# Kernel tuning notes

Measured on AMD Instinct MI355X. Metric: run time of the kernel, lower is better.

## Reference

```python
import jax, jax.numpy as jnp
import numpy as np

NV = 1_000_000   # number of 'var' nodes
NC = 500_000     # number of 'con' nodes
E = 16_000_000   # number of v2c edges (c2v is the reverse edge set)
H = 10           # n_h_feats


def setup_inputs() -> dict:
    key = jax.random.key(0)
    ks = jax.random.split(key, 24)
    s = 0.1  # weight init scale
    inp = {
        "var_c": jax.random.normal(ks[0], (NV,), jnp.float32),
        "var_x": jax.random.normal(ks[1], (NV,), jnp.float32),
        "con_b": jax.random.normal(ks[2], (NC,), jnp.float32),
        "A": jax.random.uniform(ks[3], (E,), jnp.float32),
        "src": jax.random.randint(ks[4], (E,), 0, NV, jnp.int32),
        "dst": jax.random.randint(ks[5], (E,), 0, NC, jnp.int32),
        # var_emb / con_emb Linear params
        "Wv": jax.random.normal(ks[6], (2, H), jnp.float32) * s,
        "bv": jnp.zeros((H,), jnp.float32),
        "Wc": jax.random.normal(ks[7], (1, H), jnp.float32) * s,
        "bc": jnp.zeros((H,), jnp.float32),
        # conv1 (GraphConv, shared across v2c/c2v) -- note: its output is
        # overwritten in the original forward and never reaches the output
        "W1": jax.random.normal(ks[8], (H, H), jnp.float32) * s,
        "b1": jnp.zeros((H,), jnp.float32),
        # conv2 (GraphConv, shared across v2c/c2v)
        "W2": jax.random.normal(ks[9], (H, H), jnp.float32) * s,
        "b2": jnp.zeros((H,), jnp.float32),
        # output MLP
        "Wo1": jax.random.normal(ks[10], (H, H), jnp.float32) * s,
        "bo1": jnp.zeros((H,), jnp.float32),
        "Wo2": jax.random.normal(ks[11], (H, H), jnp.float32) * s,
        "bo2": jnp.zeros((H,), jnp.float32),
        "Wo3": jax.random.normal(ks[12], (H, 1), jnp.float32) * s,
        "bo3": jnp.zeros((1,), jnp.float32),
    }
    return inp


def _gconv(x_src, W, b, s_idx, d_idx, ew, norm_src, norm_dst, n_dst):
    # DGL GraphConv, norm='both', with edge weights; in==out feats so W first.
    h = (x_src * norm_src) @ W                      # [N_src, H]
    msg = h[s_idx] * ew[:, None]                    # gather + edge weight
    agg = jax.ops.segment_sum(msg, d_idx, num_segments=n_dst)
    return agg * norm_dst + b


def reference(var_c, var_x, con_b, A, src, dst,
              Wv, bv, Wc, bc, W1, b1, W2, b2,
              Wo1, bo1, Wo2, bo2, Wo3, bo3):
    # symmetric norm from UNWEIGHTED degrees (DGL GraphConv norm='both'),
    # clamped at 1. v2c: out-deg(var), in-deg(con); c2v is the reverse.
    ones_e = jnp.ones_like(A)
    deg_v = jnp.clip(jax.ops.segment_sum(ones_e, src, num_segments=NV), 1.0)
    deg_c = jnp.clip(jax.ops.segment_sum(ones_e, dst, num_segments=NC), 1.0)
    norm_v = deg_v[:, None] ** -0.5
    norm_c = deg_c[:, None] ** -0.5

    # node embeddings
    var_feats = jnp.stack([var_c, var_x], axis=1)   # [NV, 2]
    X_var = jax.nn.relu(var_feats @ Wv + bv)        # [NV, H]
    X_con = jax.nn.relu(con_b[:, None] @ Wc + bc)   # [NC, H] (unused by convs: GraphConv ignores dst feats)

    # In the original forward, conv1 outputs (h_con / h_var) are immediately
    # overwritten by conv2 outputs (GraphConv only consumes src features),
    # so only conv2 lies on the effective compute path.
    h_con = jax.nn.relu(_gconv(X_var, W2, b2, src, dst, A, norm_v, norm_c, NC))
    h_var = jax.nn.relu(_gconv(h_con, W2, b2, dst, src, A, norm_c, norm_v, NV))

    h = jax.nn.relu(h_var @ Wo1 + bo1)
    h = jax.nn.relu(h @ Wo2 + bo2)
    logit = h @ Wo3 + bo3                           # [NV, 1]
    # dgl.readout_nodes(op='mean', ntype='var'), single graph -> [1, 1]
    return jnp.mean(logit, axis=0, keepdims=True)
```

## Files before the change

### kernel.cpp

```cpp
#include <hip/hip_runtime.h>

#define HF 10
#define ST 16
#define BST 16
#define SLC 256
#define NBINS 2048
#define VPB 512
#define TILE 12288
#define NBD 1024
#define DSH 9
#define CPB 512
#define TILED 6144


__global__ __launch_bounds__(1024) void k_hist(const int* __restrict__ idx,
                                               unsigned* __restrict__ hist,
                                               long long s_begin, long long s_end,
                                               int per, int shift) {
    __shared__ unsigned l[NBINS];
    int t = threadIdx.x, sl = blockIdx.x;
    for (int b = t; b < NBINS; b += 1024) l[b] = 0u;
    __syncthreads();
    long long s0 = s_begin + (long long)sl * per;
    long long s1 = s0 + per; if (s1 > s_end) s1 = s_end;
    for (long long i = s0 + t; i < s1; i += 1024)
        atomicAdd(&l[((unsigned)idx[i]) >> shift], 1u);
    __syncthreads();
    unsigned* out = hist + (size_t)sl * NBINS;
    for (int b = t; b < NBINS; b += 1024) out[b] = l[b];
}

__global__ void k_coltot(const unsigned* __restrict__ h, unsigned* __restrict__ colT) {
    int b = blockIdx.x * 256 + threadIdx.x;
    unsigned s = 0u;
    for (int sl = 0; sl < SLC; sl++) s += h[(size_t)sl * NBINS + b];
    colT[b] = s;
}

__global__ __launch_bounds__(1024) void k_prefix(const unsigned* __restrict__ colT,
                                                 unsigned* __restrict__ start) {
    __shared__ unsigned p[1024];
    int t = threadIdx.x;
    uint2 v = *(const uint2*)(colT + 2 * t);
    unsigned own = v.x + v.y;
    p[t] = own;
    __syncthreads();
    for (int off = 1; off < 1024; off <<= 1) {
        unsigned u = (t >= off) ? p[t - off] : 0u;
        __syncthreads();
        p[t] += u;
        __syncthreads();
    }
    unsigned e = p[t] - own;
    *(uint2*)(start + 2 * t) = make_uint2(e, e + v.x);
    if (t == 1023) start[NBINS] = p[1023];
}

__global__ void k_offs(unsigned* __restrict__ h, const unsigned* __restrict__ start) {
    int b = blockIdx.x * 256 + threadIdx.x;
    unsigned cur = start[b];
    for (int sl = 0; sl < SLC; sl++) {
        unsigned* cell = h + (size_t)sl * NBINS + b;
        unsigned v = *cell;
        *cell = cur;
        cur += v;
    }
}

__global__ __launch_bounds__(1024) void k_scatS2(
        const int* __restrict__ src, const int* __restrict__ dst,
        const float* __restrict__ A, const unsigned* __restrict__ offs,
        uint2* __restrict__ ebufS, long long E, int per) {
    __shared__ unsigned cur[NBINS];
    __shared__ unsigned th[NBINS];
    __shared__ unsigned tf[NBINS];
    __shared__ unsigned sc[1024];
    __shared__ __align__(16) uint2 buf[TILE];
    int t = threadIdx.x, sl = blockIdx.x;
    const unsigned* o = offs + (size_t)sl * NBINS;
    for (int b = t; b < NBINS; b += 1024) cur[b] = o[b];
    long long s0 = (long long)sl * per;
    long long s1 = s0 + per; if (s1 > E) s1 = E;
    for (long long tb = s0; tb < s1; tb += TILE) {
        int n = (int)((s1 - tb < (long long)TILE) ? (s1 - tb) : (long long)TILE);
        for (int b = t; b < NBINS; b += 1024) th[b] = 0u;
        __syncthreads();
        for (int i = t; i < n; i += 1024)
            atomicAdd(&th[((unsigned)src[tb + i]) >> 9], 1u);
        __syncthreads();
        unsigned a0 = th[2 * t], a1 = th[2 * t + 1];
        unsigned own = a0 + a1;
        sc[t] = own;
        __syncthreads();
        for (int off = 1; off < 1024; off <<= 1) {
            unsigned u = (t >= off) ? sc[t - off] : 0u;
            __syncthreads();
            sc[t] += u;
            __syncthreads();
        }
        unsigned ex = sc[t] - own;
        th[2 * t] = ex;     th[2 * t + 1] = ex + a0;
        tf[2 * t] = ex;     tf[2 * t + 1] = ex + a0;
        __syncthreads();
        for (int i = t; i < n; i += 1024) {
            unsigned s = (unsigned)src[tb + i], d = (unsigned)dst[tb + i];
            float a = A[tb + i];
            unsigned p = atomicAdd(&tf[s >> 9], 1u);
            buf[p] = make_uint2(((s & 511u) << 19) | d, __float_as_uint(a));
        }
        __syncthreads();
        int w = t >> 6, ln = t & 63;
        for (int b = w; b < NBINS; b += 16) {
            unsigned lo = th[b], cnt = tf[b] - lo, gb = cur[b];
            for (unsigned j = ln; j < cnt; j += 64)
                ebufS[gb + j] = buf[lo + j];
        }
        __syncthreads();
        for (int b = t; b < NBINS; b += 1024) cur[b] += tf[b] - th[b];
        __syncthreads();
    }
}

__global__ void k_cntS2(const uint2* __restrict__ ebufS, const unsigned* __restrict__ startS,
                        const float* __restrict__ var_c, const float* __restrict__ var_x,
                        float4* __restrict__ vcx, int NV) {
    __shared__ unsigned cnt[VPB];
    int t = threadIdx.x, b = blockIdx.x;
    cnt[t] = 0u; cnt[t + 256] = 0u;
    __syncthreads();
    unsigned i0 = startS[b], i1 = startS[b + 1];
    for (unsigned i = i0 + t; i < i1; i += 256)
        atomicAdd(&cnt[ebufS[i].x >> 19], 1u);
    __syncthreads();
#pragma unroll
    for (int k = 0; k < 2; k++) {
        int v = b * VPB + k * 256 + t;
        if (v < NV)
            vcx[v] = make_float4(var_c[v], var_x[v],
                                 rsqrtf(fmaxf((float)cnt[k * 256 + t], 1.0f)), 0.0f);
    }
}

__global__ __launch_bounds__(1024) void k_histD2(const uint2* __restrict__ ebufB,
                                                 const unsigned* __restrict__ startS,
                                                 unsigned* __restrict__ hist, int B0, int binsPer) {
    __shared__ unsigned l[NBINS];
    int t = threadIdx.x, sl = blockIdx.x;
    for (int b = t; b < NBINS; b += 1024) l[b] = 0u;
    __syncthreads();
    int b0 = B0 + sl * binsPer;
    unsigned i0 = startS[b0], i1 = startS[b0 + binsPer];
    for (unsigned i = i0 + t; i < i1; i += 1024)
        atomicAdd(&l[(ebufB[i].x & 0x7FFFFu) >> DSH], 1u);
    __syncthreads();
    unsigned* out = hist + (size_t)sl * NBINS;
    for (int b = t; b < NBINS; b += 1024) out[b] = l[b];
}

__global__ __launch_bounds__(1024) void k_scatD3(
        const uint2* __restrict__ ebufB, const unsigned* __restrict__ startS,
        const unsigned* __restrict__ offs, const float4* __restrict__ vcx,
        uint4* __restrict__ ebufD, int B0, int binsPer, unsigned cap) {
    __shared__ unsigned cur[NBD];
    __shared__ unsigned th[NBD], tf[NBD];
    __shared__ unsigned sc[1024];
    __shared__ __align__(16) uint4 buf[TILED];
    int t = threadIdx.x, sl = blockIdx.x;
    const unsigned* o = offs + (size_t)sl * NBINS;
    cur[t] = o[t];
    __syncthreads();
    int b0 = B0 + sl * binsPer;
    for (int bb = 0; bb < binsPer; bb++) {
        int bin = b0 + bb;
        unsigned vbase = ((unsigned)bin) << 9;
        unsigned i0 = startS[bin], i1 = startS[bin + 1];
        for (unsigned tb = i0; tb < i1; tb += TILED) {
            unsigned n = (i1 - tb < (unsigned)TILED) ? (i1 - tb) : (unsigned)TILED;
            th[t] = 0u;
            __syncthreads();
            for (unsigned i = t; i < n; i += 1024)
                atomicAdd(&th[(ebufB[tb + i].x & 0x7FFFFu) >> DSH], 1u);
            __syncthreads();
            unsigned own = th[t];
            sc[t] = own;
            __syncthreads();
            for (int off = 1; off < 1024; off <<= 1) {
                unsigned u = (t >= off) ? sc[t - off] : 0u;
                __syncthreads();
                sc[t] += u;
                __syncthreads();
            }
            unsigned ex = sc[t] - own;
            th[t] = ex; tf[t] = ex;
            __syncthreads();
            for (unsigned i = t; i < n; i += 1024) {
                uint2 kv = ebufB[tb + i];
                unsigned d = kv.x & 0x7FFFFu;
                float4 g = vcx[vbase | (kv.x >> 19)];
                unsigned p = atomicAdd(&tf[d >> DSH], 1u);
                buf[p] = make_uint4(d & (CPB - 1u),
                                    __float_as_uint(__uint_as_float(kv.y) * g.z),
                                    __float_as_uint(g.x), __float_as_uint(g.y));
            }
            __syncthreads();
            int w = t >> 6, ln = t & 63;
            for (int b = w; b < NBD; b += 16) {
                unsigned lo = th[b], cnt = tf[b] - lo, gb = cur[b];
                for (unsigned j = ln; j < cnt; j += 64)
                    if (gb + j < cap) ebufD[gb + j] = buf[lo + j];
            }
            __syncthreads();
            cur[t] += tf[t] - th[t];
            __syncthreads();
        }
    }
}

__global__ __launch_bounds__(1024) void k_scatD(const int* __restrict__ src, const int* __restrict__ dst,
                                                const float* __restrict__ A,
                                                const unsigned* __restrict__ offs,
                                                const float4* __restrict__ vcx,
                                                uint4* __restrict__ ebufD,
                                                long long s_begin, long long s_end, int per) {
    __shared__ unsigned cur[NBINS];
    int t = threadIdx.x, sl = blockIdx.x;
    const unsigned* o = offs + (size_t)sl * NBINS;
    for (int b = t; b < NBINS; b += 1024) cur[b] = o[b];
    __syncthreads();
    long long s0 = s_begin + (long long)sl * per;
    long long s1 = s0 + per; if (s1 > s_end) s1 = s_end;
    for (long long i = s0 + t; i < s1; i += 4096) {
        unsigned sv[4], dv[4]; float av[4]; bool hv[4];
#pragma unroll
        for (int j = 0; j < 4; j++) {
            long long idx = i + (long long)j * 1024;
            hv[j] = idx < s1;
            if (hv[j]) { sv[j] = (unsigned)src[idx]; dv[j] = (unsigned)dst[idx]; av[j] = A[idx]; }
            else       { sv[j] = 0u; dv[j] = 0u; av[j] = 0.0f; }
        }
        float4 g[4];
#pragma unroll
        for (int j = 0; j < 4; j++)
            if (hv[j]) g[j] = vcx[sv[j]];
#pragma unroll
        for (int j = 0; j < 4; j++) {
            if (!hv[j]) continue;
            unsigned pos = atomicAdd(&cur[dv[j] >> DSH], 1u);
            ebufD[pos] = make_uint4(dv[j] & (CPB - 1u), __float_as_uint(av[j] * g[j].z),
                                    __float_as_uint(g[j].x), __float_as_uint(g[j].y));
        }
    }
}

__global__ __launch_bounds__(256) void k_aggD(
        const uint4* __restrict__ ebufD, const unsigned* __restrict__ startD,
        const float* __restrict__ Wv, const float* __restrict__ bv,
        float* __restrict__ bufC, float* __restrict__ deg_c, int NC) {
    __shared__ float acc[CPB * HF];
    __shared__ unsigned cnt[CPB];
    int t = threadIdx.x, b = blockIdx.x;
    for (int i = t; i < CPB * HF; i += 256) acc[i] = 0.0f;
    cnt[t] = 0u; cnt[t + 256] = 0u;
    float wv0[HF], wv1[HF], bvv[HF];
#pragma unroll
    for (int h = 0; h < HF; h++) { wv0[h] = Wv[h]; wv1[h] = Wv[HF + h]; bvv[h] = bv[h]; }
    __syncthreads();
    unsigned i0 = startD[b], i1 = startD[b + 1];
    for (unsigned i = i0 + t; i < i1; i += 256) {
        uint4 kv = ebufD[i];
        unsigned dl = kv.x;
        float anv = __uint_as_float(kv.y);
        float c   = __uint_as_float(kv.z);
        float x   = __uint_as_float(kv.w);
        float* ac = acc + dl * HF;
#pragma unroll
        for (int h = 0; h < HF; h++) {
            float e = fmaxf(fmaf(c, wv0[h], fmaf(x, wv1[h], bvv[h])), 0.0f);
            atomicAdd(ac + h, anv * e);
        }
        atomicAdd(&cnt[dl], 1u);
    }
    __syncthreads();
#pragma unroll
    for (int k = 0; k < 2; k++) {
        int gid = b * CPB + k * 256 + t;
        if (gid < NC) {
            float* row = bufC + (size_t)gid * BST;
#pragma unroll
            for (int h = 0; h < HF; h++) row[h] += acc[(k * 256 + t) * HF + h];
            deg_c[gid] += (float)cnt[k * 256 + t];
        }
    }
}

__global__ void k_conT(float* __restrict__ bufC, const float* __restrict__ deg_c,
                       const float* __restrict__ W2, const float* __restrict__ b2, int NC) {
    __shared__ float sW[HF * HF], sb[HF];
    int t = threadIdx.x;
    if (t < HF * HF) sW[t] = W2[t];
    if (t < HF)      sb[t] = b2[t];
    __syncthreads();
    int i = blockIdx.x * 256 + t;
    if (i >= NC) return;
    float nc = rsqrtf(fmaxf(deg_c[i], 1.0f));
    float* row = bufC + (size_t)i * BST;
    float x[HF];
#pragma unroll
    for (int h = 0; h < HF; h++) x[h] = row[h];
#pragma unroll
    for (int j = 0; j < HF; j++) {
        float a = 0.0f;
#pragma unroll
        for (int k = 0; k < HF; k++) a = fmaf(x[k], sW[k * HF + j], a);
        row[j] = fmaxf(fmaf(a, nc, sb[j]), 0.0f) * nc;
    }
}

__global__ __launch_bounds__(256) void k_aggS(
        const uint2* __restrict__ ebufS, const unsigned* __restrict__ startS,
        const float* __restrict__ bufC, const float4* __restrict__ vcx,
        const float* __restrict__ W2, const float* __restrict__ b2,
        const float* __restrict__ Wo1, const float* __restrict__ bo1,
        const float* __restrict__ Wo2, const float* __restrict__ bo2,
        const float* __restrict__ Wo3, const float* __restrict__ bo3,
        double* __restrict__ gacc, int NV) {
    __shared__ float acc[VPB * HF];
    __shared__ float sW2[HF * HF], sb2[HF], sW1[HF * HF], sb1[HF], sWm[HF * HF], sbm[HF], sW3[HF];
    __shared__ float sb3;
    __shared__ double red[256];
    int t = threadIdx.x, b = blockIdx.x;
    for (int i = t; i < VPB * HF; i += 256) acc[i] = 0.0f;
    if (t < HF * HF) { sW2[t] = W2[t]; sW1[t] = Wo1[t]; sWm[t] = Wo2[t]; }
    if (t < HF)      { sb2[t] = b2[t]; sb1[t] = bo1[t]; sbm[t] = bo2[t]; sW3[t] = Wo3[t]; }
    if (t == 0)      sb3 = bo3[0];
    __syncthreads();
    unsigned i0 = startS[b], i1 = startS[b + 1];
    int grp = t >> 2;
    int q   = t & 3;
    int nq  = (q < 2) ? 4 : (q == 2 ? 2 : 0);
    for (unsigned base = i0; base < i1; base += 64) {
        unsigned e = base + (unsigned)grp;
        bool ok = e < i1;
        uint2 kv = ok ? ebufS[e] : make_uint2(0u, 0u);
        float4 y = make_float4(0.f, 0.f, 0.f, 0.f);
        if (ok) y = *(const float4*)(bufC + (size_t)(kv.x & 0x7FFFFu) * BST + 4 * q);
        if (ok && nq) {
            float a = __uint_as_float(kv.y);
            float* ac = acc + (kv.x >> 19) * HF + 4 * q;
            atomicAdd(ac + 0, a * y.x);
            atomicAdd(ac + 1, a * y.y);
            if (nq == 4) {
                atomicAdd(ac + 2, a * y.z);
                atomicAdd(ac + 3, a * y.w);
            }
        }
    }
    __syncthreads();
    double local = 0.0;
#pragma unroll
    for (int k = 0; k < 2; k++) {
        int v = b * VPB + k * 256 + t;
        if (v < NV) {
            float nv = vcx[v].z;
            float x[HF], hvv[HF], h1[HF], h2[HF];
#pragma unroll
            for (int h = 0; h < HF; h++) x[h] = acc[(k * 256 + t) * HF + h];
#pragma unroll
            for (int j = 0; j < HF; j++) {
                float a = 0.0f;
#pragma unroll
                for (int kk = 0; kk < HF; kk++) a = fmaf(x[kk], sW2[kk * HF + j], a);
                hvv[j] = fmaxf(fmaf(a, nv, sb2[j]), 0.0f);
            }
#pragma unroll
            for (int j = 0; j < HF; j++) {
                float a = sb1[j];
#pragma unroll
                for (int kk = 0; kk < HF; kk++) a = fmaf(hvv[kk], sW1[kk * HF + j], a);
                h1[j] = fmaxf(a, 0.0f);
            }
#pragma unroll
            for (int j = 0; j < HF; j++) {
                float a = sbm[j];
#pragma unroll
                for (int kk = 0; kk < HF; kk++) a = fmaf(h1[kk], sWm[kk * HF + j], a);
                h2[j] = fmaxf(a, 0.0f);
            }
            float logit = sb3;
#pragma unroll
            for (int kk = 0; kk < HF; kk++) logit = fmaf(h2[kk], sW3[kk], logit);
            local += (double)logit;
        }
    }
    red[t] = local;
    __syncthreads();
    for (int s = 128; s > 0; s >>= 1) {
        if (t < s) red[t] += red[t + s];
        __syncthreads();
    }
    if (t == 0) atomicAdd(gacc, red[0]);
}

__global__ void k_out(const double* __restrict__ acc, float* __restrict__ out, int NV) {
    out[0] = (float)(acc[0] / (double)NV);
}


__global__ void k_degree(const int* __restrict__ src, const int* __restrict__ dst,
                         float* __restrict__ deg_v, float* __restrict__ deg_c, int E) {
    int i = blockIdx.x * blockDim.x + threadIdx.x;
    if (i < E) {
        atomicAdd(&deg_v[src[i]], 1.0f);
        atomicAdd(&deg_c[dst[i]], 1.0f);
    }
}

__global__ void k_norm(float* __restrict__ d, int n) {
    int i = blockIdx.x * blockDim.x + threadIdx.x;
    if (i < n) d[i] = 1.0f / sqrtf(fmaxf(d[i], 1.0f));
}

__global__ void k_var_emb(const float* __restrict__ var_c, const float* __restrict__ var_x,
                          const float* __restrict__ norm_v,
                          const float* __restrict__ Wv, const float* __restrict__ bv,
                          const float* __restrict__ W2,
                          float* __restrict__ out, int NV) {
    __shared__ float sWv[2 * HF], sbv[HF], sW2[HF * HF];
    int t = threadIdx.x;
    if (t < 2 * HF) sWv[t] = Wv[t];
    if (t < HF)     sbv[t] = bv[t];
    if (t < HF * HF) sW2[t] = W2[t];
    __syncthreads();
    int i = blockIdx.x * blockDim.x + t;
    if (i >= NV) return;
    float c = var_c[i], x = var_x[i], nv = norm_v[i];
    float e[HF];
#pragma unroll
    for (int h = 0; h < HF; h++)
        e[h] = fmaxf(fmaf(c, sWv[h], fmaf(x, sWv[HF + h], sbv[h])), 0.0f) * nv;
    float* row = out + (size_t)i * ST;
#pragma unroll
    for (int j = 0; j < HF; j++) {
        float acc = 0.0f;
#pragma unroll
        for (int k = 0; k < HF; k++) acc = fmaf(e[k], sW2[k * HF + j], acc);
        row[j] = acc;
    }
}

__global__ void k_edge(const int* __restrict__ gidx, const int* __restrict__ didx,
                       const float* __restrict__ A,
                       const float* __restrict__ h, float* __restrict__ agg, int E) {
    int tid = blockIdx.x * blockDim.x + threadIdx.x;
    int e = tid / 5;
    if (e >= E) return;
    int q = tid - e * 5;
    int s = gidx[e], d = didx[e];
    float a = A[e];
    const float2 m = *(const float2*)(h + (size_t)s * ST + 2 * q);
    float* o = agg + (size_t)d * ST + 2 * q;
    atomicAdd(o,     m.x * a);
    atomicAdd(o + 1, m.y * a);
}

__global__ void k_con(float* __restrict__ buf, const float* __restrict__ norm_c,
                      const float* __restrict__ W2, const float* __restrict__ b2, int NC) {
    __shared__ float sW2[HF * HF], sb2[HF];
    int t = threadIdx.x;
    if (t < HF * HF) sW2[t] = W2[t];
    if (t < HF)      sb2[t] = b2[t];
    __syncthreads();
    int i = blockIdx.x * blockDim.x + t;
    if (i >= NC) return;
    float nc = norm_c[i];
    float* row = buf + (size_t)i * ST;
    float hc[HF];
#pragma unroll
    for (int h = 0; h < HF; h++)
        hc[h] = fmaxf(fmaf(row[h], nc, sb2[h]), 0.0f) * nc;
#pragma unroll
    for (int j = 0; j < HF; j++) {
        float acc = 0.0f;
#pragma unroll
        for (int k = 0; k < HF; k++) acc = fmaf(hc[k], sW2[k * HF + j], acc);
        row[j] = acc;
    }
}

__global__ void k_final(const float* __restrict__ agg_v, const float* __restrict__ norm_v,
                        const float* __restrict__ b2,
                        const float* __restrict__ Wo1, const float* __restrict__ bo1,
                        const float* __restrict__ Wo2, const float* __restrict__ bo2,
                        const float* __restrict__ Wo3, const float* __restrict__ bo3,
                        double* __restrict__ acc, int NV) {
    __shared__ float sb2[HF], sW1[HF * HF], sb1[HF], sW2m[HF * HF], sb2m[HF], sW3[HF];
    __shared__ float sb3;
    __shared__ double red[256];
    int t = threadIdx.x;
    if (t < HF)      sb2[t]  = b2[t];
    if (t < HF * HF) sW1[t]  = Wo1[t];
    if (t < HF)      sb1[t]  = bo1[t];
    if (t < HF * HF) sW2m[t] = Wo2[t];
    if (t < HF)      sb2m[t] = bo2[t];
    if (t < HF)      sW3[t]  = Wo3[t];
    if (t == 0)      sb3     = bo3[0];
    __syncthreads();
    int i = blockIdx.x * blockDim.x + t;
    double local = 0.0;
    if (i < NV) {
        float nv = norm_v[i];
        const float* row = agg_v + (size_t)i * ST;
        float v[HF], h1[HF], h2[HF];
#pragma unroll
        for (int h = 0; h < HF; h++) v[h] = fmaxf(fmaf(row[h], nv, sb2[h]), 0.0f);
#pragma unroll
        for (int j = 0; j < HF; j++) {
            float a = sb1[j];
#pragma unroll
            for (int k = 0; k < HF; k++) a = fmaf(v[k], sW1[k * HF + j], a);
            h1[j] = fmaxf(a, 0.0f);
        }
#pragma unroll
        for (int j = 0; j < HF; j++) {
            float a = sb2m[j];
#pragma unroll
            for (int k = 0; k < HF; k++) a = fmaf(h1[k], sW2m[k * HF + j], a);
            h2[j] = fmaxf(a, 0.0f);
        }
        float logit = sb3;
#pragma unroll
        for (int k = 0; k < HF; k++) logit = fmaf(h2[k], sW3[k], logit);
        local = (double)logit;
    }
    red[t] = local;
    __syncthreads();
    for (int s = 128; s > 0; s >>= 1) {
        if (t < s) red[t] += red[t + s];
        __syncthreads();
    }
    if (t == 0) atomicAdd(acc, red[0]);
}


extern "C" void kernel_launch(void* const* d_in, const int* in_sizes, int n_in,
                              void* d_out, int out_size, void* d_ws, size_t ws_size,
                              hipStream_t stream) {
    const float* var_c = (const float*)d_in[0];
    const float* var_x = (const float*)d_in[1];
    const float* A   = (const float*)d_in[3];
    const int*   src = (const int*)d_in[4];
    const int*   dst = (const int*)d_in[5];
    const float* Wv  = (const float*)d_in[6];
    const float* bv  = (const float*)d_in[7];
    const float* W2  = (const float*)d_in[12];
    const float* b2  = (const float*)d_in[13];
    const float* Wo1 = (const float*)d_in[14];
    const float* bo1 = (const float*)d_in[15];
    const float* Wo2 = (const float*)d_in[16];
    const float* bo2 = (const float*)d_in[17];
    const float* Wo3 = (const float*)d_in[18];
    const float* bo3 = (const float*)d_in[19];

    const int NV = in_sizes[0];
    const int NC = in_sizes[2];
    const int E  = in_sizes[3];

    long long EcMaxUsed = 0;
    auto layout_bytes = [&](int nDc, bool binchunk, size_t* offs_out) -> size_t {
        size_t off = 0;
        auto alloc = [&](size_t bytes, int slot) {
            if (offs_out) offs_out[slot] = off;
            off = (off + bytes + 255) & ~(size_t)255;
        };
        long long ec;
        if (binchunk) {
            long long vspan = (long long)(NBINS / nDc) * VPB;
            if (vspan > NV) vspan = NV;
            ec = ((long long)E * vspan) / NV + (long long)E / 64 + 1024;
            if (ec > E) ec = E;
        } else {
            ec = ((long long)E + nDc - 1) / nDc;
        }
        EcMaxUsed = ec;
        alloc((size_t)NC * BST * 4, 0);
        alloc((size_t)NV * 16, 1);
        alloc((size_t)NC * 4, 2);
        alloc((size_t)SLC * NBINS * 4, 3);
        alloc((size_t)SLC * NBINS * 4, 4);
        alloc((size_t)NBINS * 4, 5);
        alloc((size_t)(NBINS + 1) * 4, 6);
        alloc((size_t)(NBINS + 1) * 4, 7);
        alloc(8, 8);
        alloc((size_t)E * 8, 9);
        alloc((size_t)ec * 16, 10);
        return off;
    };

    int nD = 0;
    bool binc = false;
    size_t offs[11];
    for (int cand : {4, 8, 16}) {
        if (layout_bytes(cand, true, nullptr) <= ws_size) { nD = cand; binc = true; break; }
    }
    if (nD == 0) {
        for (int cand = 2; cand <= 16; cand++)
            if (layout_bytes(cand, false, nullptr) <= ws_size) { nD = cand; break; }
    }
    bool fast = (nD > 0) && (NV <= (1 << 20)) && (NC <= (1 << 19)) && (E > 0);

    char* ws = (char*)d_ws;
    if (fast) {
        layout_bytes(nD, binc, offs);
        const long long EcMax = EcMaxUsed;
        float*    bufC   = (float*)(ws + offs[0]);
        float4*   vcx    = (float4*)(ws + offs[1]);
        float*    deg_c  = (float*)(ws + offs[2]);
        unsigned* hS     = (unsigned*)(ws + offs[3]);
        unsigned* hD     = (unsigned*)(ws + offs[4]);
        unsigned* colT   = (unsigned*)(ws + offs[5]);
        unsigned* startS = (unsigned*)(ws + offs[6]);
        unsigned* startD = (unsigned*)(ws + offs[7]);
        double*   gacc   = (double*)(ws + offs[8]);
        uint2*    ebufS  = (uint2*)(ws + offs[9]);
        uint4*    ebufD  = (uint4*)(ws + offs[10]);

        const int perS = (int)(((long long)E + SLC - 1) / SLC);
        const int NB_S = (NV + VPB - 1) / VPB;
        const int NB_C = (NC + 255) >> 8;
        const int NB_C2 = (NC + CPB - 1) / CPB;

        hipMemsetAsync(bufC,  0, (size_t)NC * BST * 4, stream);
        hipMemsetAsync(deg_c, 0, (size_t)NC * 4, stream);
        hipMemsetAsync(gacc,  0, 8, stream);

        k_hist<<<SLC, 1024, 0, stream>>>(src, hS, 0, E, perS, 9);
        k_coltot<<<NBINS / 256, 256, 0, stream>>>(hS, colT);
        k_prefix<<<1, 1024, 0, stream>>>(colT, startS);
        k_offs<<<NBINS / 256, 256, 0, stream>>>(hS, startS);
        k_scatS2<<<SLC, 1024, 0, stream>>>(src, dst, A, hS, ebufS, E, perS);

        k_cntS2<<<NB_S, 256, 0, stream>>>(ebufS, startS, var_c, var_x, vcx, NV);

        if (binc) {
            const int binsChunk = NBINS / nD;
            const int binsPer   = (binsChunk + SLC - 1) / SLC;
            for (int c = 0; c < nD; c++) {
                int B0 = c * binsChunk;
                k_histD2<<<SLC, 1024, 0, stream>>>(ebufS, startS, hD, B0, binsPer);
                k_coltot<<<NBINS / 256, 256, 0, stream>>>(hD, colT);
                k_prefix<<<1, 1024, 0, stream>>>(colT, startD);
                k_offs<<<NBINS / 256, 256, 0, stream>>>(hD, startD);
                k_scatD3<<<SLC, 1024, 0, stream>>>(ebufS, startS, hD, vcx, ebufD,
                                                   B0, binsPer, (unsigned)EcMax);
                k_aggD<<<NB_C2, 256, 0, stream>>>(ebufD, startD, Wv, bv, bufC, deg_c, NC);
            }
        } else {
            const int perD = (int)((EcMax + SLC - 1) / SLC);
            for (int c = 0; c < nD; c++) {
                long long cb = (long long)c * EcMax;
                long long ce = cb + EcMax; if (ce > E) ce = E;
                k_hist<<<SLC, 1024, 0, stream>>>(dst, hD, cb, ce, perD, DSH);
                k_coltot<<<NBINS / 256, 256, 0, stream>>>(hD, colT);
                k_prefix<<<1, 1024, 0, stream>>>(colT, startD);
                k_offs<<<NBINS / 256, 256, 0, stream>>>(hD, startD);
                k_scatD<<<SLC, 1024, 0, stream>>>(src, dst, A, hD, vcx, ebufD, cb, ce, perD);
                k_aggD<<<NB_C2, 256, 0, stream>>>(ebufD, startD, Wv, bv, bufC, deg_c, NC);
            }
        }
        k_conT<<<NB_C, 256, 0, stream>>>(bufC, deg_c, W2, b2, NC);

        k_aggS<<<NB_S, 256, 0, stream>>>(ebufS, startS, bufC, vcx, W2, b2,
                                         Wo1, bo1, Wo2, bo2, Wo3, bo3, gacc, NV);
        k_out<<<1, 1, 0, stream>>>(gacc, (float*)d_out, NV);
    } else {
        const int B = 256;
        float* fbufV = (float*)ws;
        float* fbufC = (float*)(ws + (size_t)NV * ST * 4);
        float* deg_v = (float*)(ws + (size_t)(NV + NC) * ST * 4);
        float* deg_c = deg_v + NV;
        size_t acc_off = ((size_t)(NV + NC) * ST * 4 + (size_t)(NV + NC) * 4 + 7) & ~(size_t)7;
        double* acc = (double*)(ws + acc_off);

        hipMemsetAsync(deg_v, 0, (size_t)(NV + NC) * 4, stream);
        hipMemsetAsync(fbufC, 0, (size_t)NC * ST * 4, stream);
        hipMemsetAsync(acc, 0, sizeof(double), stream);

        k_degree<<<(E + B - 1) / B, B, 0, stream>>>(src, dst, deg_v, deg_c, E);
        k_norm<<<(NV + NC + B - 1) / B, B, 0, stream>>>(deg_v, NV + NC);
        k_var_emb<<<(NV + B - 1) / B, B, 0, stream>>>(var_c, var_x, deg_v, Wv, bv, W2, fbufV, NV);

        long long tE = (long long)E * 5;
        k_edge<<<(int)((tE + B - 1) / B), B, 0, stream>>>(src, dst, A, fbufV, fbufC, E);
        k_con<<<(NC + B - 1) / B, B, 0, stream>>>(fbufC, deg_c, W2, b2, NC);

        hipMemsetAsync(fbufV, 0, (size_t)NV * ST * 4, stream);
        k_edge<<<(int)((tE + B - 1) / B), B, 0, stream>>>(dst, src, A, fbufC, fbufV, E);

        k_final<<<(NV + B - 1) / B, B, 0, stream>>>(fbufV, deg_v, b2, Wo1, bo1, Wo2, bo2, Wo3, bo3, acc, NV);
        k_out<<<1, 1, 0, stream>>>(acc, (float*)d_out, NV);
    }
}
```

Baseline: 2.626 ms.

## Widen destination bins, merge per-slice bins into tiles, use wave-shuffle scan

Destination bucketing now uses 512 bins of 1024 constraints instead of 1024 bins of 512, and the in-block scatter tile grows. k_scatD4 handles all of a slice's source bins as one contiguous range and recovers each edge's source bin by comparing against the bin boundaries. It replaces the 1024-wide barrier-heavy Hillis-Steele scan with a wave-level shuffle scan and flattens the write-out so each thread copies records directly. k_aggD now has 1024 constraints per block (40 KB shared accumulator), masks the local index itself, and exits early on empty blocks. The goal is fewer barriers, fewer underfilled tiles and more coalesced writes, at the cost of more shared memory per block (possibly lower occupancy) and a per-edge boundary search loop.

New measurement: 2.477 ms. 5.7% less time.

```diff
diff --git a/kernel.cpp b/kernel.cpp
--- a/kernel.cpp
+++ b/kernel.cpp
@@ -7,10 +7,10 @@
 #define NBINS 2048
 #define VPB 512
 #define TILE 12288
-#define NBD 1024
-#define DSH 9
-#define CPB 512
-#define TILED 6144
+#define NBD 512
+#define DSH 10
+#define CPB 1024
+#define TILED 7424
 
 
 __global__ __launch_bounds__(1024) void k_hist(const int* __restrict__ idx,
@@ -143,13 +143,17 @@
 
 __global__ __launch_bounds__(1024) void k_histD2(const uint2* __restrict__ ebufB,
                                                  const unsigned* __restrict__ startS,
-                                                 unsigned* __restrict__ hist, int B0, int binsPer) {
+                                                 unsigned* __restrict__ hist,
+                                                 int B0, int binsPer, int binsChunk) {
     __shared__ unsigned l[NBINS];
     int t = threadIdx.x, sl = blockIdx.x;
     for (int b = t; b < NBINS; b += 1024) l[b] = 0u;
     __syncthreads();
     int b0 = B0 + sl * binsPer;
-    unsigned i0 = startS[b0], i1 = startS[b0 + binsPer];
+    int bend = b0 + binsPer;
+    if (bend > B0 + binsChunk) bend = B0 + binsChunk;
+    unsigned i0 = 0u, i1 = 0u;
+    if (b0 < bend) { i0 = startS[b0]; i1 = startS[bend]; }
     for (unsigned i = i0 + t; i < i1; i += 1024)
         atomicAdd(&l[(ebufB[i].x & 0x7FFFFu) >> DSH], 1u);
     __syncthreads();
@@ -157,62 +161,70 @@
     for (int b = t; b < NBINS; b += 1024) out[b] = l[b];
 }
 
-__global__ __launch_bounds__(1024) void k_scatD3(
+__global__ __launch_bounds__(1024) void k_scatD4(
         const uint2* __restrict__ ebufB, const unsigned* __restrict__ startS,
         const unsigned* __restrict__ offs, const float4* __restrict__ vcx,
-        uint4* __restrict__ ebufD, int B0, int binsPer, unsigned cap) {
-    __shared__ unsigned cur[NBD];
-    __shared__ unsigned th[NBD], tf[NBD];
-    __shared__ unsigned sc[1024];
+        uint4* __restrict__ ebufD, int B0, int binsPer, int binsChunk, unsigned cap) {
+    __shared__ unsigned cur[NBD], th[NBD], tf[NBD];
+    __shared__ unsigned ws[16];
+    __shared__ unsigned bnd[16];
     __shared__ __align__(16) uint4 buf[TILED];
     int t = threadIdx.x, sl = blockIdx.x;
+    int b0 = B0 + sl * binsPer;
+    int bend = b0 + binsPer;
+    if (bend > B0 + binsChunk) bend = B0 + binsChunk;
+    int binsEff = bend - b0;
+    if (binsEff <= 0) return;
     const unsigned* o = offs + (size_t)sl * NBINS;
-    cur[t] = o[t];
-    __syncthreads();
-    int b0 = B0 + sl * binsPer;
-    for (int bb = 0; bb < binsPer; bb++) {
-        int bin = b0 + bb;
-        unsigned vbase = ((unsigned)bin) << 9;
-        unsigned i0 = startS[bin], i1 = startS[bin + 1];
-        for (unsigned tb = i0; tb < i1; tb += TILED) {
-            unsigned n = (i1 - tb < (unsigned)TILED) ? (i1 - tb) : (unsigned)TILED;
-            th[t] = 0u;
-            __syncthreads();
-            for (unsigned i = t; i < n; i += 1024)
-                atomicAdd(&th[(ebufB[tb + i].x & 0x7FFFFu) >> DSH], 1u);
-            __syncthreads();
-            unsigned own = th[t];
-            sc[t] = own;
-            __syncthreads();
-            for (int off = 1; off < 1024; off <<= 1) {
-                unsigned u = (t >= off) ? sc[t - off] : 0u;
-                __syncthreads();
-                sc[t] += u;
-                __syncthreads();
-            }
-            unsigned ex = sc[t] - own;
-            th[t] = ex; tf[t] = ex;
-            __syncthreads();
-            for (unsigned i = t; i < n; i += 1024) {
-                uint2 kv = ebufB[tb + i];
-                unsigned d = kv.x & 0x7FFFFu;
-                float4 g = vcx[vbase | (kv.x >> 19)];
-                unsigned p = atomicAdd(&tf[d >> DSH], 1u);
-                buf[p] = make_uint4(d & (CPB - 1u),
-                                    __float_as_uint(__uint_as_float(kv.y) * g.z),
-                                    __float_as_uint(g.x), __float_as_uint(g.y));
-            }
-            __syncthreads();
-            int w = t >> 6, ln = t & 63;
-            for (int b = w; b < NBD; b += 16) {
-                unsigned lo = th[b], cnt = tf[b] - lo, gb = cur[b];
-                for (unsigned j = ln; j < cnt; j += 64)
-                    if (gb + j < cap) ebufD[gb + j] = buf[lo + j];
-            }
-            __syncthreads();
-            cur[t] += tf[t] - th[t];
-            __syncthreads();
-        }
+    if (t < NBD) cur[t] = o[t];
+    if (t <= binsEff) bnd[t] = startS[b0 + t];
+    __syncthreads();
+    unsigned r0 = bnd[0], r1 = bnd[binsEff];
+    for (unsigned tb = r0; tb < r1; tb += TILED) {
+        unsigned n = (r1 - tb < (unsigned)TILED) ? (r1 - tb) : (unsigned)TILED;
+        if (t < NBD) th[t] = 0u;
+        __syncthreads();
+        for (unsigned i = t; i < n; i += 1024)
+            atomicAdd(&th[(ebufB[tb + i].x & 0x7FFFFu) >> DSH], 1u);
+        __syncthreads();
+        unsigned own = (t < NBD) ? th[t] : 0u;
+        unsigned v = own;
+#pragma unroll
+        for (int d = 1; d < 64; d <<= 1) {
+            unsigned u = __shfl_up(v, (unsigned)d, 64);
+            if ((t & 63) >= d) v += u;
+        }
+        if ((t & 63) == 63 && t < NBD) ws[t >> 6] = v;
+        __syncthreads();
+        if (t == 0) {
+            unsigned run = 0u;
+#pragma unroll
+            for (int w = 0; w < NBD / 64; w++) { unsigned x = ws[w]; ws[w] = run; run += x; }
+        }
+        __syncthreads();
+        if (t < NBD) { unsigned ex = v - own + ws[t >> 6]; th[t] = ex; tf[t] = ex; }
+        __syncthreads();
+        for (unsigned i = t; i < n; i += 1024) {
+            unsigned gi = tb + i;
+            uint2 kv = ebufB[gi];
+            unsigned d = kv.x & 0x7FFFFu;
+            unsigned sb = 0u;
+            for (int j = 1; j < binsEff; j++) sb += (gi >= bnd[j]) ? 1u : 0u;
+            float4 g = vcx[(((unsigned)b0 + sb) << 9) | (kv.x >> 19)];
+            unsigned p = atomicAdd(&tf[d >> DSH], 1u);
+            buf[p] = make_uint4(d, __float_as_uint(__uint_as_float(kv.y) * g.z),
+                                __float_as_uint(g.x), __float_as_uint(g.y));
+        }
+        __syncthreads();
+        for (unsigned p = t; p < n; p += 1024) {
+            uint4 rec = buf[p];
+            unsigned b = rec.x >> DSH;
+            unsigned pos = cur[b] + (p - th[b]);
+            if (pos < cap) ebufD[pos] = rec;
+        }
+        __syncthreads();
+        if (t < NBD) cur[t] += tf[t] - th[t];
+        __syncthreads();
     }
 }
 
@@ -246,7 +258,7 @@
         for (int j = 0; j < 4; j++) {
             if (!hv[j]) continue;
             unsigned pos = atomicAdd(&cur[dv[j] >> DSH], 1u);
-            ebufD[pos] = make_uint4(dv[j] & (CPB - 1u), __float_as_uint(av[j] * g[j].z),
+            ebufD[pos] = make_uint4(dv[j], __float_as_uint(av[j] * g[j].z),
                                     __float_as_uint(g[j].x), __float_as_uint(g[j].y));
         }
     }
@@ -259,16 +271,18 @@
     __shared__ float acc[CPB * HF];
     __shared__ unsigned cnt[CPB];
     int t = threadIdx.x, b = blockIdx.x;
+    unsigned i0 = startD[b], i1 = startD[b + 1];
+    if (i0 >= i1) return;
     for (int i = t; i < CPB * HF; i += 256) acc[i] = 0.0f;
-    cnt[t] = 0u; cnt[t + 256] = 0u;
+#pragma unroll
+    for (int k = 0; k < CPB / 256; k++) cnt[k * 256 + t] = 0u;
     float wv0[HF], wv1[HF], bvv[HF];
 #pragma unroll
     for (int h = 0; h < HF; h++) { wv0[h] = Wv[h]; wv1[h] = Wv[HF + h]; bvv[h] = bv[h]; }
     __syncthreads();
-    unsigned i0 = startD[b], i1 = startD[b + 1];
     for (unsigned i = i0 + t; i < i1; i += 256) {
         uint4 kv = ebufD[i];
-        unsigned dl = kv.x;
+        unsigned dl = kv.x & (CPB - 1u);
         float anv = __uint_as_float(kv.y);
         float c   = __uint_as_float(kv.z);
         float x   = __uint_as_float(kv.w);
@@ -282,7 +296,7 @@
     }
     __syncthreads();
 #pragma unroll
-    for (int k = 0; k < 2; k++) {
+    for (int k = 0; k < CPB / 256; k++) {
         int gid = b * CPB + k * 256 + t;
         if (gid < NC) {
             float* row = bufC + (size_t)gid * BST;
@@ -646,12 +660,12 @@
             const int binsPer   = (binsChunk + SLC - 1) / SLC;
             for (int c = 0; c < nD; c++) {
                 int B0 = c * binsChunk;
-                k_histD2<<<SLC, 1024, 0, stream>>>(ebufS, startS, hD, B0, binsPer);
+                k_histD2<<<SLC, 1024, 0, stream>>>(ebufS, startS, hD, B0, binsPer, binsChunk);
                 k_coltot<<<NBINS / 256, 256, 0, stream>>>(hD, colT);
                 k_prefix<<<1, 1024, 0, stream>>>(colT, startD);
                 k_offs<<<NBINS / 256, 256, 0, stream>>>(hD, startD);
-                k_scatD3<<<SLC, 1024, 0, stream>>>(ebufS, startS, hD, vcx, ebufD,
-                                                   B0, binsPer, (unsigned)EcMax);
+                k_scatD4<<<SLC, 1024, 0, stream>>>(ebufS, startS, hD, vcx, ebufD,
+                                                   B0, binsPer, binsChunk, (unsigned)EcMax);
                 k_aggD<<<NB_C2, 256, 0, stream>>>(ebufD, startD, Wv, bv, bufC, deg_c, NC);
             }
         } else {
```
